# Optimization experiments

Measured on AMD Instinct MI355X. Metric: run time of the kernel, lower is better.

The kernel has to match this reference:

```python
import jax, jax.numpy as jnp
import numpy as np

B, G, D, L, F = 64, 1024, 256, 2, 1024  # batch, graph_size, embed_dim, n_layers, ffn hidden
NEG = -30.0  # mask fill value when evaluate=False (training path)


def _uniform(key, shape, fan):
    stdv = 1.0 / np.sqrt(fan)
    return jax.random.uniform(key, shape, jnp.float32, -stdv, stdv)


def setup_inputs() -> dict:
    key = jax.random.key(0)
    ks = jax.random.split(key, 12)
    x = jax.random.normal(ks[0], (B, G, D), jnp.float32)
    mask = jax.random.randint(ks[1], (B, G), 0, 2, jnp.int32)  # 1 = attention blocked
    # weights stored as [in, out] (transposed vs torch Linear); same math.
    Wq = _uniform(ks[2], (L, D, D), D)
    Wk = _uniform(ks[3], (L, D, D), D)
    Wv = _uniform(ks[4], (L, D, D), D)
    Wo = _uniform(ks[5], (L, D, D), D)
    bo = _uniform(ks[6], (L, D), D)
    Wf1 = _uniform(ks[7], (L, D, F), D)
    bf1 = _uniform(ks[8], (L, F), F)
    Wf2 = _uniform(ks[9], (L, F, D), F)
    bf2 = _uniform(ks[10], (L, D), D)
    return {"x": x, "mask": mask, "Wq": Wq, "Wk": Wk, "Wv": Wv,
            "Wo": Wo, "bo": bo, "Wf1": Wf1, "bf1": bf1, "Wf2": Wf2, "bf2": bf2}


def reference(x, mask, Wq, Wk, Wv, Wo, bo, Wf1, bf1, Wf2, bf2):
    # GraphAttentionEncoder with n_heads=1 (key_dim = val_dim = embed_dim).
    m = mask.astype(bool)[:, None, :]            # [B,1,G] -> broadcast over query dim
    norm = 1.0 / jnp.sqrt(jnp.asarray(D, x.dtype))
    h = x
    for l in range(L):
        # --- MultiHeadAttention with residual (SkipConnection) ---
        q = h @ Wq[l]                            # [B,G,D]
        k = h @ Wk[l]
        v = h @ Wv[l]
        c = norm * jnp.einsum('bqd,bkd->bqk', q, k)   # [B,G,G]
        c = jnp.where(m, NEG, c)                 # masked fill (-30, evaluate=False)
        a = jax.nn.softmax(c, axis=-1)
        a = jnp.where(m, 0.0, a)                 # post-softmax zeroing of masked weights
        heads = jnp.einsum('bqk,bkd->bqd', a, v)
        h = h + heads @ Wo[l] + bo[l]
        # --- feed-forward with residual (SkipConnection_Linear) ---
        h = h + jax.nn.relu(h @ Wf1[l] + bf1[l]) @ Wf2[l] + bf2[l]
    return h, h.mean(axis=1)
```

## Files before the change

kernel.cpp:

```cpp
#include <hip/hip_runtime.h>
#include <hip/hip_bf16.h>

#define Bdim 64
#define Gdim 1024
#define Ddim 256
#define Fdim 1024

typedef short s8v __attribute__((ext_vector_type(8)));
typedef short s4v __attribute__((ext_vector_type(4)));
typedef float f4v __attribute__((ext_vector_type(4)));

__device__ __forceinline__ float bf2f(short s){
  return __uint_as_float(((unsigned)(unsigned short)s) << 16);
}
__device__ __forceinline__ short f2bf(float f){
  unsigned u = __float_as_uint(f);
  u = u + 0x7fffu + ((u >> 16) & 1u);
  return (short)(u >> 16);
}
__device__ __forceinline__ s8v ld8(const short* p){ return *(const s8v*)p; }

#define MFMA_BF16(a,b,c) __builtin_amdgcn_mfma_f32_16x16x32_bf16((a),(b),(c),0,0,0)

#define GLDS16(gp, lp) __builtin_amdgcn_global_load_lds( \
    (const __attribute__((address_space(1))) void*)(gp), \
    (__attribute__((address_space(3))) void*)(lp), 16, 0, 0)

__global__ __launch_bounds__(256) void detect_dtype(const unsigned* __restrict__ x,
                                                    int* __restrict__ flag){
  __shared__ int cnt[256];
  int c = 0;
  #pragma unroll
  for (int j=0;j<4;j++){
    unsigned u = x[threadIdx.x*4 + j];
    int e = (u >> 7) & 0xFF;
    c += (e >= 100 && e <= 140) ? 1 : 0;
  }
  cnt[threadIdx.x] = c;
  __syncthreads();
  if (threadIdx.x == 0){
    int s = 0;
    for (int i=0;i<256;i++) s += cnt[i];
    flag[0] = (s >= 512) ? 0 : 1;
  }
}

__global__ void diag_ws(void* o, float v, const int* __restrict__ flag){
  if (threadIdx.x == 0){
    if (flag[0]){ ((float*)o)[0] = v; ((float*)o)[16777216] = v; }
    else        { ((short*)o)[0] = f2bf(v); ((short*)o)[16777216] = f2bf(v); }
  }
}

__global__ __launch_bounds__(256) void cast_in(const void* __restrict__ x,
                                               float* __restrict__ h32,
                                               const int* __restrict__ flag){
  size_t i = ((size_t)blockIdx.x * 256 + threadIdx.x) * 8;
  if (flag[0]){
    const float* xf = (const float*)x;
    #pragma unroll
    for (int j=0;j<8;j++) h32[i+j] = xf[i+j];
  } else {
    s8v v = ld8((const short*)x + i);
    #pragma unroll
    for (int j=0;j<8;j++) h32[i+j] = bf2f(v[j]);
  }
}

__global__ __launch_bounds__(256) void transpose_w(const void* __restrict__ src,
                                                   short* __restrict__ dh, int R, int C,
                                                   const int* __restrict__ flag,
                                                   int dzs, int dbase){
  __shared__ short th[32][33];
  int fl = flag[0];
  size_t soff = (size_t)blockIdx.z * R * C;
  size_t doff = (size_t)dbase + (size_t)blockIdx.z * dzs;
  int c0 = blockIdx.x*32, r0 = blockIdx.y*32;
  int tx = threadIdx.x, ty = threadIdx.y;
  #pragma unroll
  for (int i=ty;i<32;i+=8){
    size_t idx = soff + (size_t)(r0+i)*C + (c0+tx);
    float w = fl ? ((const float*)src)[idx] : bf2f(((const short*)src)[idx]);
    th[i][tx] = f2bf(w);
  }
  __syncthreads();
  #pragma unroll
  for (int i=ty;i<32;i+=8)
    dh[doff + (size_t)(c0+i)*R + (r0+tx)] = th[tx][i];
}

__global__ __launch_bounds__(256) void bias_prep(const void* __restrict__ bo,
                                                 const void* __restrict__ bf1,
                                                 const void* __restrict__ bf2,
                                                 float* __restrict__ biasf,
                                                 const int* __restrict__ flag){
  int fl = flag[0];
  int i = blockIdx.x*256 + threadIdx.x;
  const void* src; int idx;
  if (i < 512){ src = bo; idx = i; }
  else if (i < 2560){ src = bf1; idx = i - 512; }
  else { src = bf2; idx = i - 2560; }
  biasf[i] = fl ? ((const float*)src)[idx] : bf2f(((const short*)src)[idx]);
}

template<int AM, int EPI>
__global__ __launch_bounds__(256) void gemm_t(
    const void* __restrict__ Ap, const short* __restrict__ Bh,
    const float* __restrict__ bias, float* __restrict__ hout,
    short* __restrict__ outb, int N, int K, int lda, int ldb, int Mrows)
{
  __shared__ short As[2][128*32];
  __shared__ short Bs[2][128*32];
  __shared__ short Asl[(AM==2)?2:1][(AM==2)?128*32:1];
  const int tid = threadIdx.x;
  const int lane = tid & 63, wave = tid >> 6;
  const int quad = lane >> 4, l16 = lane & 15;
  const int m0 = blockIdx.x * 128, n0 = blockIdx.y * 128;
  const int wr = wave >> 1, wc = wave & 1;
  const int roff = ((quad ^ (l16 & 3)) << 3);
  f4v acc[4][4];
  #pragma unroll
  for (int i=0;i<4;i++)
    #pragma unroll
    for (int j=0;j<4;j++) acc[i][j] = f4v{0.f,0.f,0.f,0.f};

  int rr[2], ss[2], dst[2];
  #pragma unroll
  for (int i=0;i<2;i++){
    int idx = i*256 + tid;
    rr[i] = idx >> 2;
    ss[i] = (idx & 3) ^ (rr[i] & 3);
    dst[i] = idx * 8;
  }

  auto stageB = [&](int buf, int k0){
    #pragma unroll
    for (int i=0;i<2;i++)
      GLDS16(Bh + (size_t)(n0 + rr[i])*ldb + k0 + ss[i]*8, &Bs[buf][dst[i]]);
  };
  auto stageA0 = [&](int buf, int k0){
    #pragma unroll
    for (int i=0;i<2;i++)
      GLDS16((const short*)Ap + (size_t)(m0 + rr[i])*lda + k0 + ss[i]*8, &As[buf][dst[i]]);
  };

  const int T = K >> 5;
  int cur = 0;
  float4 pf0a, pf0b, pf1a, pf1b;
  stageB(0, 0);
  if (AM == 0){
    stageA0(0, 0);
  } else {
    #pragma unroll
    for (int i=0;i<2;i++){
      const float* ap = (const float*)Ap + (size_t)(m0 + rr[i])*lda + ss[i]*8;
      float4 a = *(const float4*)ap, b = *(const float4*)(ap + 4);
      float fv[8] = {a.x,a.y,a.z,a.w,b.x,b.y,b.z,b.w};
      s8v hi, lo;
      #pragma unroll
      for (int j=0;j<8;j++) hi[j] = f2bf(fv[j]);
      *(s8v*)(&As[0][dst[i]]) = hi;
      if (AM == 2){
        #pragma unroll
        for (int j=0;j<8;j++) lo[j] = f2bf(fv[j] - bf2f(hi[j]));
        *(s8v*)(&Asl[0][dst[i]]) = lo;
      }
    }
  }

  for (int t = 0; t < T; ++t){
    __syncthreads();
    const int nk = (t + 1) << 5;
    if (t + 1 < T){
      stageB(cur ^ 1, nk);
      if (AM == 0){
        stageA0(cur ^ 1, nk);
      } else {
        const float* ap0 = (const float*)Ap + (size_t)(m0 + rr[0])*lda + nk + ss[0]*8;
        const float* ap1 = (const float*)Ap + (size_t)(m0 + rr[1])*lda + nk + ss[1]*8;
        pf0a = *(const float4*)ap0; pf0b = *(const float4*)(ap0 + 4);
        pf1a = *(const float4*)ap1; pf1b = *(const float4*)(ap1 + 4);
      }
    }
    s8v ah[4], al[4], bh[4];
    #pragma unroll
    for (int q=0;q<4;q++){
      ah[q] = ld8(&As[cur][(wr*64 + q*16 + l16)*32 + roff]);
      bh[q] = ld8(&Bs[cur][(wc*64 + q*16 + l16)*32 + roff]);
      if (AM == 2) al[q] = ld8(&Asl[cur][(wr*64 + q*16 + l16)*32 + roff]);
    }
    __builtin_amdgcn_s_setprio(1);
    #pragma unroll
    for (int ti=0;ti<4;ti++)
      #pragma unroll
      for (int tj=0;tj<4;tj++){
        acc[ti][tj] = MFMA_BF16(ah[ti], bh[tj], acc[ti][tj]);
        if (AM == 2) acc[ti][tj] = MFMA_BF16(al[ti], bh[tj], acc[ti][tj]);
      }
    __builtin_amdgcn_s_setprio(0);
    if (AM != 0 && t + 1 < T){
      float fv0[8] = {pf0a.x,pf0a.y,pf0a.z,pf0a.w,pf0b.x,pf0b.y,pf0b.z,pf0b.w};
      float fv1[8] = {pf1a.x,pf1a.y,pf1a.z,pf1a.w,pf1b.x,pf1b.y,pf1b.z,pf1b.w};
      s8v hi0, hi1, lo0, lo1;
      #pragma unroll
      for (int j=0;j<8;j++){ hi0[j] = f2bf(fv0[j]); hi1[j] = f2bf(fv1[j]); }
      *(s8v*)(&As[cur^1][dst[0]]) = hi0;
      *(s8v*)(&As[cur^1][dst[1]]) = hi1;
      if (AM == 2){
        #pragma unroll
        for (int j=0;j<8;j++){
          lo0[j] = f2bf(fv0[j] - bf2f(hi0[j]));
          lo1[j] = f2bf(fv1[j] - bf2f(hi1[j]));
        }
        *(s8v*)(&Asl[cur^1][dst[0]]) = lo0;
        *(s8v*)(&Asl[cur^1][dst[1]]) = lo1;
      }
    }
    cur ^= 1;
  }
  #pragma unroll
  for (int tj=0;tj<4;tj++){
    int col = n0 + wc*64 + tj*16 + l16;
    float bs = (EPI==1 || EPI==4) ? (bias ? bias[col] : 0.f) : 0.f;
    #pragma unroll
    for (int ti=0;ti<4;ti++){
      #pragma unroll
      for (int r=0;r<4;r++){
        int row = m0 + wr*64 + ti*16 + quad*4 + r;
        float v = acc[ti][tj][r];
        if (EPI == 0){
          outb[(size_t)row * N + col] = f2bf(v);
        } else if (EPI == 1){
          v += bs; v = v > 0.f ? v : 0.f;
          outb[(size_t)row * N + col] = f2bf(v);
        } else if (EPI == 4){
          size_t idx = (size_t)row * N + col;
          hout[idx] += v + bs;
        } else {
          int sec = col >> 8, c = col & 255;
          if (sec == 0)      outb[(size_t)row*256 + c] = f2bf(v);
          else if (sec == 1) (outb + (size_t)Mrows*256)[(size_t)row*256 + c] = f2bf(v);
          else {
            int bb = row >> 10, g = row & 1023;
            (outb + (size_t)2*Mrows*256)[(size_t)bb*262144 + (size_t)c*1024 + g] = f2bf(v);
          }
        }
      }
    }
  }
}

__global__ __launch_bounds__(512, 2) void flash_attn(
    const short* __restrict__ Q, const short* __restrict__ Kmat,
    const short* __restrict__ Vt, const int* __restrict__ mask,
    short* __restrict__ H)
{
  __shared__ short Ks[2][64*256];
  __shared__ short Vs[2][256*64];
  __shared__ short Ps[8][16*72];
  const int tid = threadIdx.x;
  const int lane = tid & 63, wave = tid >> 6;
  const int quad = lane >> 4, l16 = lane & 15;
  const int bid = blockIdx.x;
  const int b  = (bid & 7) + ((bid >> 6) << 3);
  const int qt = (bid >> 3) & 7;
  const short* Qb  = Q    + (size_t)b*Gdim*Ddim;
  const short* Kb  = Kmat + (size_t)b*Gdim*Ddim;
  const short* Vtb = Vt   + (size_t)b*Ddim*Gdim;
  const int qbase = qt*128 + wave*16;

  auto stage = [&](int buf, int k0){
    #pragma unroll
    for (int i=0;i<4;i++){
      int idx = i*512 + tid;
      int r = idx >> 5, g = idx & 31;
      GLDS16(Kb + (size_t)(k0 + r)*Ddim + ((g ^ (r & 7)) << 3), &Ks[buf][idx*8]);
    }
    #pragma unroll
    for (int i=0;i<4;i++){
      int idx = i*512 + tid;
      int d = idx >> 3, g = idx & 7;
      GLDS16(Vtb + (size_t)d*Gdim + k0 + ((g ^ (d & 7)) << 3), &Vs[buf][idx*8]);
    }
  };

  s8v qf[8];
  #pragma unroll
  for (int s=0;s<8;s++)
    qf[s] = ld8(Qb + (size_t)(qbase + l16)*Ddim + s*32 + quad*8);
  float mrow[4], lsum[4];
  #pragma unroll
  for (int r=0;r<4;r++){ mrow[r] = -1e9f; lsum[r] = 0.f; }
  f4v O[16];
  #pragma unroll
  for (int t=0;t<16;t++) O[t] = f4v{0.f,0.f,0.f,0.f};
  short* Pw = Ps[wave];

  stage(0, 0);
  __syncthreads();
  int cur = 0;
  for (int kt=0; kt<16; kt++){
    const int k0 = kt*64;
    if (kt < 15) stage(cur^1, k0 + 64);
    int mk[4];
    #pragma unroll
    for (int tj=0;tj<4;tj++) mk[tj] = mask[b*Gdim + k0 + tj*16 + l16];
    f4v sc[4];
    #pragma unroll
    for (int tj=0;tj<4;tj++) sc[tj] = f4v{0.f,0.f,0.f,0.f};
    const short* Kc = &Ks[cur][0];
    __builtin_amdgcn_s_setprio(1);
    #pragma unroll
    for (int st=0; st<8; st++){
      #pragma unroll
      for (int tj=0;tj<4;tj++){
        int row = tj*16 + l16;
        s8v kb = ld8(Kc + row*256 + (((st*4 + quad) ^ (row & 7)) << 3));
        sc[tj] = MFMA_BF16(qf[st], kb, sc[tj]);
      }
    }
    __builtin_amdgcn_s_setprio(0);
    float al[4]; bool need = false;
    #pragma unroll
    for (int r=0;r<4;r++){
      float mx = -1e9f;
      #pragma unroll
      for (int tj=0;tj<4;tj++){
        float v = sc[tj][r] * 0.0625f;
        if (mk[tj]) v = -30.f;
        sc[tj][r] = v;
        mx = fmaxf(mx, v);
      }
      #pragma unroll
      for (int mm=1; mm<16; mm<<=1) mx = fmaxf(mx, __shfl_xor(mx, mm));
      float mn = fmaxf(mrow[r], mx);
      al[r] = __expf(mrow[r] - mn);
      need |= (al[r] < 1.f);
      mrow[r] = mn;
      float ps = 0.f;
      #pragma unroll
      for (int tj=0;tj<4;tj++){
        float e = __expf(sc[tj][r] - mn);
        ps += e;
        sc[tj][r] = mk[tj] ? 0.f : e;
      }
      lsum[r] = lsum[r]*al[r] + ps;
    }
    if (__any(need)){
      #pragma unroll
      for (int t=0;t<16;t++)
        #pragma unroll
        for (int r=0;r<4;r++) O[t][r] *= al[r];
    }
    #pragma unroll
    for (int tj=0;tj<4;tj++)
      #pragma unroll
      for (int r=0;r<4;r++)
        Pw[(quad*4 + r)*72 + tj*16 + l16] = f2bf(sc[tj][r]);
    asm volatile("s_waitcnt lgkmcnt(0)" ::: "memory");
    __builtin_amdgcn_sched_barrier(0);
    const short* Vc = &Vs[cur][0];
    __builtin_amdgcn_s_setprio(1);
    #pragma unroll
    for (int st=0; st<2; st++){
      s8v pa = ld8(&Pw[l16*72 + st*32 + quad*8]);
      #pragma unroll
      for (int tt=0; tt<16; tt++){
        int d = tt*16 + l16;
        s8v vb = ld8(Vc + d*64 + (((st*4 + quad) ^ (d & 7)) << 3));
        O[tt] = MFMA_BF16(pa, vb, O[tt]);
      }
    }
    __builtin_amdgcn_s_setprio(0);
    __syncthreads();
    cur ^= 1;
  }
  float dn[4];
  #pragma unroll
  for (int r=0;r<4;r++){
    float s = lsum[r];
    #pragma unroll
    for (int mm=1; mm<16; mm<<=1) s += __shfl_xor(s, mm);
    dn[r] = fmaxf(s, 1e-30f);
  }
  #pragma unroll
  for (int t=0;t<16;t++){
    #pragma unroll
    for (int r=0;r<4;r++){
      int row = qbase + quad*4 + r;
      int col = t*16 + l16;
      H[((size_t)b*Gdim + row)*Ddim + col] = f2bf(O[t][r] / dn[r]);
    }
  }
}

__global__ __launch_bounds__(256) void mean_partial(const float* __restrict__ h32,
                                                    float* __restrict__ part){
  int b = blockIdx.x, c = blockIdx.y, d = threadIdx.x;
  float s = 0.f;
  for (int g = c*64; g < c*64 + 64; g++)
    s += h32[((size_t)b*Gdim + g)*Ddim + d];
  part[(b*16 + c)*Ddim + d] = s;
}
__global__ __launch_bounds__(256) void mean_final_dyn(const float* __restrict__ part,
                                                      void* __restrict__ out,
                                                      const int* __restrict__ flag){
  int i = blockIdx.x*256 + threadIdx.x;
  int b = i >> 8, d = i & 255;
  float s = 0.f;
  #pragma unroll
  for (int c=0;c<16;c++) s += part[(b*16 + c)*Ddim + d];
  s *= (1.f/1024.f);
  if (flag[0]) ((float*)out)[16777216 + i] = s;
  else         ((short*)out)[16777216 + i] = f2bf(s);
}
__global__ __launch_bounds__(256) void store_h(const float* __restrict__ h32,
                                               void* __restrict__ out,
                                               const int* __restrict__ flag){
  size_t i = (size_t)blockIdx.x*256 + threadIdx.x;
  if (flag[0]) ((float*)out)[i] = h32[i];
  else         ((short*)out)[i] = f2bf(h32[i]);
}

extern "C" void kernel_launch(void* const* d_in, const int* in_sizes, int n_in,
                              void* d_out, int out_size, void* d_ws, size_t ws_size,
                              hipStream_t stream)
{
  const void* xs  = d_in[0];
  const int*  mask= (const int*)d_in[1];
  const void* Wq  = d_in[2];
  const void* Wk  = d_in[3];
  const void* Wv  = d_in[4];
  const void* Wo  = d_in[5];
  const void* bo  = d_in[6];
  const void* Wf1 = d_in[7];
  const void* bf1 = d_in[8];
  const void* Wf2 = d_in[9];
  const void* bf2 = d_in[10];

  const size_t W_ALL = 786432 + 262144 + 1048576 + 1048576 + 12288;
  const size_t BASE  = 256 + 67108864;
  int CB;
  if      (ws_size >= BASE + 134217728ull + W_ALL) CB = 64;
  else if (ws_size >= BASE +  67108864ull + W_ALL) CB = 32;
  else if (ws_size >= BASE +  33554432ull + W_ALL) CB = 16;
  else CB = 0;

  char* p = (char*)d_ws;
  int* flag = (int*)p; p += 256;
  detect_dtype<<<1, 256, 0, stream>>>((const unsigned*)xs, flag);
  if (CB == 0){
    diag_ws<<<1, 64, 0, stream>>>(d_out, 2000.f + (float)(ws_size >> 20), flag);
    return;
  }
  const int M = CB * 1024, nch = 64 / CB;
  float* h32 = (float*)p; p += 67108864;
  char* arena = p;        p += (size_t)CB * 2097152;
  short* WqkvT = (short*)p; p += 786432;
  short* WoT   = (short*)p; p += 262144;
  short* Wf1T  = (short*)p; p += 1048576;
  short* Wf2T  = (short*)p; p += 1048576;
  float* biasf = (float*)p; p += 12288;
  float* part  = (float*)arena;

  short* Qc  = (short*)arena;
  short* Kc  = Qc + (size_t)M*256;
  short* Vtc = Qc + (size_t)2*M*256;
  short* Hc  = Qc + (size_t)3*M*256;
  short* Tc  = Qc;

  cast_in<<<8192, 256, 0, stream>>>(xs, h32, flag);
  dim3 tb(32,8);
  transpose_w<<<dim3(8,8,2),  tb, 0, stream>>>(Wq,  WqkvT, 256, 256,  flag, 196608, 0);
  transpose_w<<<dim3(8,8,2),  tb, 0, stream>>>(Wk,  WqkvT, 256, 256,  flag, 196608, 65536);
  transpose_w<<<dim3(8,8,2),  tb, 0, stream>>>(Wv,  WqkvT, 256, 256,  flag, 196608, 131072);
  transpose_w<<<dim3(8,8,2),  tb, 0, stream>>>(Wo,  WoT,   256, 256,  flag, 65536, 0);
  transpose_w<<<dim3(32,8,2), tb, 0, stream>>>(Wf1, Wf1T,  256, 1024, flag, 262144, 0);
  transpose_w<<<dim3(8,32,2), tb, 0, stream>>>(Wf2, Wf2T,  1024, 256, flag, 262144, 0);
  bias_prep<<<12, 256, 0, stream>>>(bo, bf1, bf2, biasf, flag);

  for (int c=0; c<nch; c++){
    float* hc = h32 + (size_t)c*M*256;
    const int* mc = mask + (size_t)c*M;
    for (int l=0; l<2; l++){
      gemm_t<1,5><<<dim3(M/128,6), 256, 0, stream>>>(hc, WqkvT + l*196608, nullptr,
                                                     nullptr, Qc, 768, 256, 256, 256, M);
      flash_attn<<<dim3(8*CB), 512, 0, stream>>>(Qc, Kc, Vtc, mc, Hc);
      gemm_t<0,4><<<dim3(M/128,2), 256, 0, stream>>>(Hc, WoT + l*65536, biasf + l*256,
                                                     hc, nullptr, 256, 256, 256, 256, M);
      gemm_t<2,1><<<dim3(M/128,8), 256, 0, stream>>>(hc, Wf1T + l*262144, biasf + 512 + l*1024,
                                                     nullptr, Tc, 1024, 256, 256, 256, M);
      gemm_t<0,4><<<dim3(M/128,2), 256, 0, stream>>>(Tc, Wf2T + l*262144, biasf + 2560 + l*256,
                                                     hc, nullptr, 256, 1024, 1024, 1024, M);
    }
  }
  mean_partial<<<dim3(64,16), 256, 0, stream>>>(h32, part);
  store_h<<<65536, 256, 0, stream>>>(h32, d_out, flag);
  mean_final_dyn<<<64, 256, 0, stream>>>(part, d_out, flag);
}
```

Baseline: 1.174 ms.

## Write V row-major then transpose separately; fuse output store with mean partials

```diff
diff --git a/kernel.cpp b/kernel.cpp
--- a/kernel.cpp
+++ b/kernel.cpp
@@ -87,6 +87,22 @@
   #pragma unroll
   for (int i=ty;i<32;i+=8)
     dh[doff + (size_t)(c0+i)*R + (r0+tx)] = th[tx][i];
+}
+
+__global__ __launch_bounds__(256) void transpose_v(const short* __restrict__ src,
+                                                   short* __restrict__ dst){
+  __shared__ short th[32][33];
+  const short* s = src + (size_t)blockIdx.z * 262144;
+  short* dd      = dst + (size_t)blockIdx.z * 262144;
+  int d0 = blockIdx.x*32, g0 = blockIdx.y*32;
+  int tx = threadIdx.x, ty = threadIdx.y;
+  #pragma unroll
+  for (int i=ty;i<32;i+=8)
+    th[i][tx] = s[(size_t)(g0+i)*256 + d0 + tx];
+  __syncthreads();
+  #pragma unroll
+  for (int i=ty;i<32;i+=8)
+    dd[(size_t)(d0+i)*1024 + g0 + tx] = th[tx][i];
 }
 
 __global__ __launch_bounds__(256) void bias_prep(const void* __restrict__ bo,
@@ -240,10 +256,7 @@
           int sec = col >> 8, c = col & 255;
           if (sec == 0)      outb[(size_t)row*256 + c] = f2bf(v);
           else if (sec == 1) (outb + (size_t)Mrows*256)[(size_t)row*256 + c] = f2bf(v);
-          else {
-            int bb = row >> 10, g = row & 1023;
-            (outb + (size_t)2*Mrows*256)[(size_t)bb*262144 + (size_t)c*1024 + g] = f2bf(v);
-          }
+          else               (outb + (size_t)3*Mrows*256)[(size_t)row*256 + c] = f2bf(v);
         }
       }
     }
@@ -394,12 +407,20 @@
   }
 }
 
-__global__ __launch_bounds__(256) void mean_partial(const float* __restrict__ h32,
-                                                    float* __restrict__ part){
+__global__ __launch_bounds__(256) void store_mean(const float* __restrict__ h32,
+                                                  void* __restrict__ out,
+                                                  float* __restrict__ part,
+                                                  const int* __restrict__ flag){
   int b = blockIdx.x, c = blockIdx.y, d = threadIdx.x;
+  int fl = flag[0];
   float s = 0.f;
-  for (int g = c*64; g < c*64 + 64; g++)
-    s += h32[((size_t)b*Gdim + g)*Ddim + d];
+  for (int g = c*64; g < c*64 + 64; g++){
+    size_t idx = ((size_t)b*Gdim + g)*Ddim + d;
+    float v = h32[idx];
+    s += v;
+    if (fl) ((float*)out)[idx] = v;
+    else    ((short*)out)[idx] = f2bf(v);
+  }
   part[(b*16 + c)*Ddim + d] = s;
 }
 __global__ __launch_bounds__(256) void mean_final_dyn(const float* __restrict__ part,
@@ -413,13 +434,6 @@
   s *= (1.f/1024.f);
   if (flag[0]) ((float*)out)[16777216 + i] = s;
   else         ((short*)out)[16777216 + i] = f2bf(s);
-}
-__global__ __launch_bounds__(256) void store_h(const float* __restrict__ h32,
-                                               void* __restrict__ out,
-                                               const int* __restrict__ flag){
-  size_t i = (size_t)blockIdx.x*256 + threadIdx.x;
-  if (flag[0]) ((float*)out)[i] = h32[i];
-  else         ((short*)out)[i] = f2bf(h32[i]);
 }
 
 extern "C" void kernel_launch(void* const* d_in, const int* in_sizes, int n_in,
@@ -485,6 +499,7 @@
     for (int l=0; l<2; l++){
       gemm_t<1,5><<<dim3(M/128,6), 256, 0, stream>>>(hc, WqkvT + l*196608, nullptr,
                                                      nullptr, Qc, 768, 256, 256, 256, M);
+      transpose_v<<<dim3(8,32,CB), tb, 0, stream>>>(Hc, Vtc);
       flash_attn<<<dim3(8*CB), 512, 0, stream>>>(Qc, Kc, Vtc, mc, Hc);
       gemm_t<0,4><<<dim3(M/128,2), 256, 0, stream>>>(Hc, WoT + l*65536, biasf + l*256,
                                                      hc, nullptr, 256, 256, 256, 256, M);
@@ -494,7 +509,6 @@
                                                      hc, nullptr, 256, 1024, 1024, 1024, M);
     }
   }
-  mean_partial<<<dim3(64,16), 256, 0, stream>>>(h32, part);
-  store_h<<<65536, 256, 0, stream>>>(h32, d_out, flag);
+  store_mean<<<dim3(64,16), 256, 0, stream>>>(h32, d_out, part, flag);
   mean_final_dyn<<<64, 256, 0, stream>>>(part, d_out, flag);
 }
```

Result: faster. 1.148 ms (-2.3%).
